# Kernel tuning notes

Hardware: AMD Instinct MI355X
Metric: run time of the kernel (lower is better)

## Reference

```python
import jax, jax.numpy as jnp
import numpy as np

B, T, D = 2, 2048, 1024
H, DK = 16, 64          # num_heads, head_dim (expand_v=1 -> d_v == d_k)
K = 4                    # short conv kernel size
EPS = 1e-5               # gated RMSNorm eps


def setup_inputs() -> dict:
    key = jax.random.key(0)
    ks = jax.random.split(key, 12)
    s = lambda d: d ** -0.5
    return {
        "x": jax.random.normal(ks[0], (B, T, D), jnp.float32),
        "Wq": jax.random.normal(ks[1], (D, H * DK), jnp.float32) * s(D),
        "Wk": jax.random.normal(ks[2], (D, H * DK), jnp.float32) * s(D),
        "Wv": jax.random.normal(ks[3], (D, H * DK), jnp.float32) * s(D),
        "Wa": jax.random.normal(ks[4], (D, H), jnp.float32) * s(D),
        "Wb": jax.random.normal(ks[5], (D, H), jnp.float32) * s(D),
        "Wg": jax.random.normal(ks[6], (D, H * DK), jnp.float32) * s(D),
        "Wo": jax.random.normal(ks[7], (H * DK, D), jnp.float32) * s(H * DK),
        "conv_q": jax.random.normal(ks[8], (H * DK, K), jnp.float32) * s(K),
        "conv_k": jax.random.normal(ks[9], (H * DK, K), jnp.float32) * s(K),
        "conv_v": jax.random.normal(ks[10], (H * DK, K), jnp.float32) * s(K),
        "A_log": jnp.log(jax.random.uniform(ks[11], (H,), jnp.float32, 1.0, 16.0)),
        "dt_bias": jnp.full((H,), 0.5, jnp.float32),
        "rms_w": jnp.ones((DK,), jnp.float32),
    }


def _short_conv(x, w):
    # causal depthwise conv1d (no bias) + silu; x: [B,T,C], w: [C,K]
    kk = w.shape[1]
    xp = jnp.pad(x, ((0, 0), (kk - 1, 0), (0, 0))).transpose(0, 2, 1)  # [B,C,T+K-1]
    y = jax.lax.conv_general_dilated(xp, w[:, None, :], (1,), 'VALID',
                                     feature_group_count=w.shape[0])
    return jax.nn.silu(y.transpose(0, 2, 1))


def _l2norm(x):
    return x * jax.lax.rsqrt(jnp.sum(x * x, -1, keepdims=True) + 1e-6)


def _gated_delta_rule(q, k, v, g, beta):
    # q,k,v: [B,T,H,Dk], g,beta: [B,T,H]; gated delta-rule linear attention
    scale = q.shape[-1] ** -0.5
    q = _l2norm(q) * scale
    k = _l2norm(k)
    qs, ks_, vs, gs, bs = (jnp.moveaxis(a, 1, 0) for a in (q, k, v, g, beta))
    h0 = jnp.zeros((q.shape[0], q.shape[2], q.shape[3], v.shape[3]), q.dtype)

    def step(h, t):
        qt, kt, vt, gt, bt = t
        h = h * jnp.exp(gt)[..., None, None]                      # decay state
        v_adj = (vt - jnp.einsum('bhk,bhkv->bhv', kt, h)) * bt[..., None]
        h = h + kt[..., None] * v_adj[:, :, None, :]              # rank-1 delta update
        ot = jnp.einsum('bhk,bhkv->bhv', qt, h)
        return h, ot

    _, o = jax.lax.scan(step, h0, (qs, ks_, vs, gs, bs))
    return jnp.moveaxis(o, 0, 1)  # [B,T,H,Dv]


def reference(x, Wq, Wk, Wv, Wa, Wb, Wg, Wo, conv_q, conv_k, conv_v, A_log, dt_bias, rms_w):
    q = _short_conv(x @ Wq, conv_q).reshape(B, T, H, DK)
    k = _short_conv(x @ Wk, conv_k).reshape(B, T, H, DK)
    v = _short_conv(x @ Wv, conv_v).reshape(B, T, H, DK)
    g = -jnp.exp(A_log) * jax.nn.softplus(x @ Wa + dt_bias)   # [B,T,H] log-decay
    beta = jax.nn.sigmoid(x @ Wb)                             # [B,T,H]
    o = _gated_delta_rule(q, k, v, g, beta)                   # [B,T,H,DK]
    gate = (x @ Wg).reshape(B, T, H, DK)
    o = o * jax.lax.rsqrt(jnp.mean(o * o, -1, keepdims=True) + EPS) * rms_w
    o = o * jax.nn.silu(gate)                                 # gated RMSNorm
    return o.reshape(B, T, H * DK) @ Wo
```

## Files before the change

### kernel.cpp

```cpp
#include <hip/hip_runtime.h>
#include <hip/hip_bf16.h>
#include <math.h>
#include <stdint.h>

#define BB 2
#define TT 2048
#define DD 1024
#define HH 16
#define DK 64
#define HD 1024
#define NC 32
#define CL 64
#define PAD 68
#define VS 16

typedef short bf16x8 __attribute__((ext_vector_type(8)));
typedef float f32x4 __attribute__((ext_vector_type(4)));
typedef unsigned short u16x8 __attribute__((ext_vector_type(8)));
typedef unsigned short u16x4 __attribute__((ext_vector_type(4)));

#define GAS __attribute__((address_space(1)))
#define LAS __attribute__((address_space(3)))

#define DOT4(a, b) ((a).x*(b).x + (a).y*(b).y + (a).z*(b).z + (a).w*(b).w)

#define OUT16(acc, kf, wv) \
    acc[0][0] += kf.x * wv.x; acc[0][1] += kf.x * wv.y; acc[0][2] += kf.x * wv.z; acc[0][3] += kf.x * wv.w; \
    acc[1][0] += kf.y * wv.x; acc[1][1] += kf.y * wv.y; acc[1][2] += kf.y * wv.z; acc[1][3] += kf.y * wv.w; \
    acc[2][0] += kf.z * wv.x; acc[2][1] += kf.z * wv.y; acc[2][2] += kf.z * wv.z; acc[2][3] += kf.z * wv.w; \
    acc[3][0] += kf.w * wv.x; acc[3][1] += kf.w * wv.y; acc[3][2] += kf.w * wv.z; acc[3][3] += kf.w * wv.w;

#define WSUB(c, hv) \
    acc[0][0] -= wa0.c * hv.x; acc[0][1] -= wa0.c * hv.y; acc[0][2] -= wa0.c * hv.z; acc[0][3] -= wa0.c * hv.w; \
    acc[1][0] -= wa1.c * hv.x; acc[1][1] -= wa1.c * hv.y; acc[1][2] -= wa1.c * hv.z; acc[1][3] -= wa1.c * hv.w; \
    acc[2][0] -= wa2.c * hv.x; acc[2][1] -= wa2.c * hv.y; acc[2][2] -= wa2.c * hv.z; acc[2][3] -= wa2.c * hv.w; \
    acc[3][0] -= wa3.c * hv.x; acc[3][1] -= wa3.c * hv.y; acc[3][2] -= wa3.c * hv.z; acc[3][3] -= wa3.c * hv.w;

#define ACC16(c, wv) \
    acc[0][0] += sa0.c * wv.x; acc[0][1] += sa0.c * wv.y; acc[0][2] += sa0.c * wv.z; acc[0][3] += sa0.c * wv.w; \
    acc[1][0] += sa1.c * wv.x; acc[1][1] += sa1.c * wv.y; acc[1][2] += sa1.c * wv.z; acc[1][3] += sa1.c * wv.w; \
    acc[2][0] += sa2.c * wv.x; acc[2][1] += sa2.c * wv.y; acc[2][2] += sa2.c * wv.z; acc[2][3] += sa2.c * wv.w; \
    acc[3][0] += sa3.c * wv.x; acc[3][1] += sa3.c * wv.y; acc[3][2] += sa3.c * wv.z; acc[3][3] += sa3.c * wv.w;

__device__ __forceinline__ float sigmoidf_(float x) { return 1.0f / (1.0f + expf(-x)); }
__device__ __forceinline__ float siluf_(float x) { return x * sigmoidf_(x); }

__device__ __forceinline__ unsigned short f2bf(float f) {
    unsigned int u = __builtin_bit_cast(unsigned int, f);
    u = (u + 0x7fffu + ((u >> 16) & 1u)) >> 16;
    return (unsigned short)u;
}

__global__ __launch_bounds__(256) void castx_k(const float* __restrict__ src,
                                               unsigned short* __restrict__ dst) {
    const size_t idx = (size_t)blockIdx.x * 256 + threadIdx.x;
    float4 a = *(const float4*)&src[idx * 8];
    float4 b = *(const float4*)&src[idx * 8 + 4];
    u16x8 o;
    o[0] = f2bf(a.x); o[1] = f2bf(a.y); o[2] = f2bf(a.z); o[3] = f2bf(a.w);
    o[4] = f2bf(b.x); o[5] = f2bf(b.y); o[6] = f2bf(b.z); o[7] = f2bf(b.w);
    *(u16x8*)&dst[idx * 8] = o;
}

__global__ __launch_bounds__(256) void castw_k(const float* __restrict__ W,
                                               unsigned short* __restrict__ Wt) {
    __shared__ float t_s[64][65];
    const int tid = threadIdx.x;
    const int rr = tid >> 4;
    const int cc = tid & 15;
    const int r0 = blockIdx.y * 64;
    const int c0 = blockIdx.x * 64;
#pragma unroll
    for (int i = 0; i < 4; ++i) {
        const int row = rr + i * 16;
        float4 v = *(const float4*)&W[(size_t)(r0 + row) * 1024 + c0 + cc * 4];
        t_s[row][cc * 4 + 0] = v.x;
        t_s[row][cc * 4 + 1] = v.y;
        t_s[row][cc * 4 + 2] = v.z;
        t_s[row][cc * 4 + 3] = v.w;
    }
    __syncthreads();
#pragma unroll
    for (int i = 0; i < 4; ++i) {
        const int nr = rr + i * 16;
        u16x4 o;
#pragma unroll
        for (int d = 0; d < 4; ++d) o[d] = f2bf(t_s[cc * 4 + d][nr]);
        *(u16x4*)&Wt[(size_t)(c0 + nr) * 1024 + r0 + cc * 4] = o;
    }
}

__global__ __launch_bounds__(256) void tw_k(const float* __restrict__ Wa,
                                            const float* __restrict__ Wb,
                                            float* __restrict__ Wt) {
    const int o = blockIdx.x;
    const int h = o & 15;
    const float* W = (o < 16) ? Wa : Wb;
    const int tid = threadIdx.x;
    float4 v;
    v.x = W[(size_t)(tid * 4 + 0) * HH + h];
    v.y = W[(size_t)(tid * 4 + 1) * HH + h];
    v.z = W[(size_t)(tid * 4 + 2) * HH + h];
    v.w = W[(size_t)(tid * 4 + 3) * HH + h];
    *(float4*)&Wt[(size_t)o * DD + tid * 4] = v;
}

__global__ __launch_bounds__(256) void gemm_bf16_k(const unsigned short* __restrict__ A,
                                                   const unsigned short* __restrict__ Bt,
                                                   float* __restrict__ C,
                                                   int M, int N, int Kd) {
    __shared__ unsigned short a_s[128 * 32];
    __shared__ unsigned short b_s[128 * 32];

    const int tid = threadIdx.x;
    const int wave = tid >> 6;
    const int lane = tid & 63;
    const int m0 = blockIdx.y * 128;
    const int n0 = blockIdx.x * 128;

    const int quad = lane >> 4;
    const int l16 = lane & 15;
    const int wr = wave >> 1;
    const int wc = wave & 1;

    const int srow = lane >> 2;
    const int sseg = lane & 3;

    f32x4 acc[4][4];
#pragma unroll
    for (int i = 0; i < 4; ++i)
#pragma unroll
        for (int j = 0; j < 4; ++j) acc[i][j] = (f32x4){0.f, 0.f, 0.f, 0.f};

    for (int k0 = 0; k0 < Kd; k0 += 32) {
        __syncthreads();
#pragma unroll
        for (int c = 0; c < 2; ++c) {
            const int region = wave * 2 + c;
            const int r0t = region * 16;
            const int ra = r0t + srow;
            const unsigned short* ga = A + (size_t)(m0 + ra) * Kd + k0 + sseg * 8;
            const unsigned short* gb = Bt + (size_t)(n0 + ra) * Kd + k0 + sseg * 8;
            __builtin_amdgcn_global_load_lds((const GAS unsigned int*)ga,
                                             (LAS unsigned int*)&a_s[r0t * 32], 16, 0, 0);
            __builtin_amdgcn_global_load_lds((const GAS unsigned int*)gb,
                                             (LAS unsigned int*)&b_s[r0t * 32], 16, 0, 0);
        }
        __syncthreads();

        bf16x8 af[4], bfr[4];
#pragma unroll
        for (int i = 0; i < 4; ++i)
            af[i] = *(const bf16x8*)&a_s[(wr * 64 + i * 16 + l16) * 32 + quad * 8];
#pragma unroll
        for (int j = 0; j < 4; ++j)
            bfr[j] = *(const bf16x8*)&b_s[(wc * 64 + j * 16 + l16) * 32 + quad * 8];
#pragma unroll
        for (int i = 0; i < 4; ++i)
#pragma unroll
            for (int j = 0; j < 4; ++j)
                acc[i][j] = __builtin_amdgcn_mfma_f32_16x16x32_bf16(af[i], bfr[j], acc[i][j], 0, 0, 0);
    }

#pragma unroll
    for (int i = 0; i < 4; ++i)
#pragma unroll
        for (int j = 0; j < 4; ++j) {
            const int col = n0 + wc * 64 + j * 16 + l16;
#pragma unroll
            for (int r = 0; r < 4; ++r) {
                const int row = m0 + wr * 64 + i * 16 + quad * 4 + r;
                C[(size_t)row * N + col] = acc[i][j][r];
            }
        }
}

__global__ __launch_bounds__(256) void gemm_qkvg_k(const unsigned short* __restrict__ A,
                                                   const unsigned short* __restrict__ Bt,
                                                   float* __restrict__ Oq,
                                                   float* __restrict__ Ok,
                                                   float* __restrict__ Ov,
                                                   float* __restrict__ Og) {
    __shared__ unsigned short a_s[128 * 32];
    __shared__ unsigned short b_s[128 * 32];

    const int tid = threadIdx.x;
    const int wave = tid >> 6;
    const int lane = tid & 63;
    const int m0 = blockIdx.y * 128;
    const int n0 = blockIdx.x * 128;

    const int quad = lane >> 4;
    const int l16 = lane & 15;
    const int wr = wave >> 1;
    const int wc = wave & 1;

    const int srow = lane >> 2;
    const int sseg = lane & 3;

    f32x4 acc[4][4];
#pragma unroll
    for (int i = 0; i < 4; ++i)
#pragma unroll
        for (int j = 0; j < 4; ++j) acc[i][j] = (f32x4){0.f, 0.f, 0.f, 0.f};

    for (int k0 = 0; k0 < DD; k0 += 32) {
        __syncthreads();
#pragma unroll
        for (int c = 0; c < 2; ++c) {
            const int region = wave * 2 + c;
            const int r0t = region * 16;
            const int ra = r0t + srow;
            const unsigned short* ga = A + (size_t)(m0 + ra) * DD + k0 + sseg * 8;
            const unsigned short* gb = Bt + (size_t)(n0 + ra) * DD + k0 + sseg * 8;
            __builtin_amdgcn_global_load_lds((const GAS unsigned int*)ga,
                                             (LAS unsigned int*)&a_s[r0t * 32], 16, 0, 0);
            __builtin_amdgcn_global_load_lds((const GAS unsigned int*)gb,
                                             (LAS unsigned int*)&b_s[r0t * 32], 16, 0, 0);
        }
        __syncthreads();

        bf16x8 af[4], bfr[4];
#pragma unroll
        for (int i = 0; i < 4; ++i)
            af[i] = *(const bf16x8*)&a_s[(wr * 64 + i * 16 + l16) * 32 + quad * 8];
#pragma unroll
        for (int j = 0; j < 4; ++j)
            bfr[j] = *(const bf16x8*)&b_s[(wc * 64 + j * 16 + l16) * 32 + quad * 8];
#pragma unroll
        for (int i = 0; i < 4; ++i)
#pragma unroll
            for (int j = 0; j < 4; ++j)
                acc[i][j] = __builtin_amdgcn_mfma_f32_16x16x32_bf16(af[i], bfr[j], acc[i][j], 0, 0, 0);
    }

    float* Cd = (n0 < 1024) ? Oq : (n0 < 2048) ? Ok : (n0 < 3072) ? Ov : Og;
    const int nl = n0 & 1023;
#pragma unroll
    for (int i = 0; i < 4; ++i)
#pragma unroll
        for (int j = 0; j < 4; ++j) {
            const int col = nl + wc * 64 + j * 16 + l16;
#pragma unroll
            for (int r = 0; r < 4; ++r) {
                const int row = m0 + wr * 64 + i * 16 + quad * 4 + r;
                Cd[(size_t)row * HD + col] = acc[i][j][r];
            }
        }
}

__global__ __launch_bounds__(256) void gbeta_k(const float* __restrict__ x,
                                               const float* __restrict__ Wt,
                                               const float* __restrict__ A_log,
                                               const float* __restrict__ dt_bias,
                                               float* __restrict__ g,
                                               float* __restrict__ beta) {
    __shared__ __align__(16) float xs[8][DD];
    const int r0 = blockIdx.x * 8;
    const int tid = threadIdx.x;

#pragma unroll
    for (int i = 0; i < 8; ++i) {
        const int f = tid + i * 256;
        const int r = f >> 8;
        const int col = (f & 255) * 4;
        *(float4*)&xs[r][col] = *(const float4*)&x[((size_t)r0 + r) * DD + col];
    }
    __syncthreads();

    const int out = tid >> 3;
    const int part = tid & 7;
    const int h = out & 15;
    const float* Wrow = Wt + (size_t)out * DD;

    float a0 = 0, a1 = 0, a2 = 0, a3 = 0, a4 = 0, a5 = 0, a6 = 0, a7 = 0;
#pragma unroll 4
    for (int i = 0; i < 32; ++i) {
        const int d = i * 32 + part * 4;
        const float4 wv = *(const float4*)&Wrow[d];
        float4 x0 = *(const float4*)&xs[0][d];
        float4 x1 = *(const float4*)&xs[1][d];
        float4 x2 = *(const float4*)&xs[2][d];
        float4 x3 = *(const float4*)&xs[3][d];
        float4 x4 = *(const float4*)&xs[4][d];
        float4 x5 = *(const float4*)&xs[5][d];
        float4 x6 = *(const float4*)&xs[6][d];
        float4 x7 = *(const float4*)&xs[7][d];
        a0 += DOT4(x0, wv); a1 += DOT4(x1, wv);
        a2 += DOT4(x2, wv); a3 += DOT4(x3, wv);
        a4 += DOT4(x4, wv); a5 += DOT4(x5, wv);
        a6 += DOT4(x6, wv); a7 += DOT4(x7, wv);
    }
#pragma unroll
    for (int s = 1; s <= 4; s <<= 1) {
        a0 += __shfl_xor(a0, s); a1 += __shfl_xor(a1, s);
        a2 += __shfl_xor(a2, s); a3 += __shfl_xor(a3, s);
        a4 += __shfl_xor(a4, s); a5 += __shfl_xor(a5, s);
        a6 += __shfl_xor(a6, s); a7 += __shfl_xor(a7, s);
    }

    if (part == 0) {
        float sv[8] = {a0, a1, a2, a3, a4, a5, a6, a7};
        if (out < 16) {
            const float ae = -expf(A_log[h]);
            const float db = dt_bias[h];
#pragma unroll
            for (int r = 0; r < 8; ++r) {
                float v = sv[r] + db;
                float sp = (v > 20.0f) ? v : log1pf(expf(v));
                g[((size_t)r0 + r) * HH + h] = ae * sp;
            }
        } else {
#pragma unroll
            for (int r = 0; r < 8; ++r)
                beta[((size_t)r0 + r) * HH + h] = sigmoidf_(sv[r]);
        }
    }
}

__global__ __launch_bounds__(64) void stage_k(const float* __restrict__ q_pre,
                                              const float* __restrict__ k_pre,
                                              const float* __restrict__ cq,
                                              const float* __restrict__ ck,
                                              const float* __restrict__ g,
                                              float* __restrict__ Qc,
                                              float* __restrict__ Kc,
                                              float* __restrict__ bcum) {
    const int blk = blockIdx.x;
    const int bh = blk >> 5;
    const int c = blk & 31;
    const int b = bh >> 4;
    const int h = bh & 15;
    const int lane = threadIdx.x;
    const int ch = h * DK + lane;

    const float4 wq4 = *(const float4*)&cq[ch * 4];
    const float4 wk4 = *(const float4*)&ck[ch * 4];

    float qw0 = 0, qw1 = 0, qw2 = 0, kw0 = 0, kw1 = 0, kw2 = 0;
    {
        const int t0 = c * CL;
        if (t0 - 3 >= 0) { size_t bi = ((size_t)b * TT + t0 - 3) * HD + ch; qw0 = q_pre[bi]; kw0 = k_pre[bi]; }
        if (t0 - 2 >= 0) { size_t bi = ((size_t)b * TT + t0 - 2) * HD + ch; qw1 = q_pre[bi]; kw1 = k_pre[bi]; }
        if (t0 - 1 >= 0) { size_t bi = ((size_t)b * TT + t0 - 1) * HD + ch; qw2 = q_pre[bi]; kw2 = k_pre[bi]; }
    }
    float* Qo = Qc + (size_t)blk * 4096;
    float* Ko = Kc + (size_t)blk * 4096;

    for (int tt = 0; tt < CL; ++tt) {
        const int t = c * CL + tt;
        const size_t bi = ((size_t)b * TT + t) * HD + ch;
        const float qc_ = q_pre[bi];
        const float kc_ = k_pre[bi];
        float qa = qw0 * wq4.x + qw1 * wq4.y + qw2 * wq4.z + qc_ * wq4.w;
        float ka = kw0 * wk4.x + kw1 * wk4.y + kw2 * wk4.z + kc_ * wk4.w;
        qw0 = qw1; qw1 = qw2; qw2 = qc_;
        kw0 = kw1; kw1 = kw2; kw2 = kc_;
        qa = siluf_(qa);
        ka = siluf_(ka);
        float qs2 = qa * qa, ks2 = ka * ka;
#pragma unroll
        for (int s = 32; s > 0; s >>= 1) {
            qs2 += __shfl_xor(qs2, s);
            ks2 += __shfl_xor(ks2, s);
        }
        Qo[tt * 64 + lane] = qa * rsqrtf(qs2 + 1e-6f) * 0.125f;
        Ko[tt * 64 + lane] = ka * rsqrtf(ks2 + 1e-6f);
    }

    float cum = g[((size_t)b * TT + c * CL + lane) * HH + h];
#pragma unroll
    for (int s = 1; s < 64; s <<= 1) {
        float u = __shfl_up(cum, s);
        if (lane >= s) cum += u;
    }
    bcum[(size_t)blk * 64 + lane] = cum;
}

__global__ __launch_bounds__(256) void prep_k(const float* __restrict__ Kc,
                                              const float* __restrict__ v_pre,
                                              const float* __restrict__ cv,
                                              const float* __restrict__ bcum,
                                              const float* __restrict__ bbuf,
                                              float* __restrict__ Wv,
                                              float* __restrict__ Wk) {
    __shared__ __align__(16) float k_s[CL * PAD];
    __shared__ __align__(16) float wv_s[CL * PAD];
    __shared__ __align__(16) float wk_s[CL * PAD];
    __shared__ __align__(16) float A_s[CL * PAD];
    __shared__ float T_s[4][16 * 17];
    __shared__ float b_s[CL], beta_s[CL], bk_s[CL];

    const int blk = blockIdx.x;
    const int bh = blk >> 5;
    const int c = blk & 31;
    const int b = bh >> 4;
    const int h = bh & 15;
    const int tid = threadIdx.x;

    if (tid < 64) {
        float bv = bcum[(size_t)blk * 64 + tid];
        float be = bbuf[((size_t)b * TT + c * CL + tid) * HH + h];
        b_s[tid] = bv;
        beta_s[tid] = be;
        bk_s[tid] = be * __expf(bv);
    }
    __syncthreads();

    {
        const float4* Kg = (const float4*)(Kc + (size_t)blk * 4096);
#pragma unroll
        for (int i = 0; i < 4; ++i) {
            int f = tid + i * 256;
            int t = f >> 4;
            int d = t * PAD + (f & 15) * 4;
            float4 kv = Kg[f];
            *(float4*)&k_s[d] = kv;
            float sk = bk_s[t];
            *(float4*)&wk_s[d] = make_float4(kv.x * sk, kv.y * sk, kv.z * sk, kv.w * sk);
        }
    }

    {
        const int lane = tid & 63;
        const int q4 = tid >> 6;
        const int ch = h * DK + lane;
        const float4 wv4 = *(const float4*)&cv[ch * 4];
        const int T0 = c * CL + q4 * 16;
        float w0 = 0, w1 = 0, w2 = 0;
        if (T0 - 3 >= 0) w0 = v_pre[((size_t)b * TT + T0 - 3) * HD + ch];
        if (T0 - 2 >= 0) w1 = v_pre[((size_t)b * TT + T0 - 2) * HD + ch];
        if (T0 - 1 >= 0) w2 = v_pre[((size_t)b * TT + T0 - 1) * HD + ch];
#pragma unroll 1
        for (int i = 0; i < 16; ++i) {
            const int t = T0 + i;
            const float vc_ = v_pre[((size_t)b * TT + t) * HD + ch];
            float va = w0 * wv4.x + w1 * wv4.y + w2 * wv4.z + vc_ * wv4.w;
            w0 = w1; w1 = w2; w2 = vc_;
            va = siluf_(va);
            wv_s[(q4 * 16 + i) * PAD + lane] = va * beta_s[q4 * 16 + i];
        }
    }
    __syncthreads();

    {
        const int t0 = (tid >> 4) * 4, s0 = (tid & 15) * 4;
        float acc[4][4] = {};
        for (int kk = 0; kk < 64; kk += 4) {
            float4 ta0 = *(const float4*)&k_s[(t0 + 0) * PAD + kk];
            float4 ta1 = *(const float4*)&k_s[(t0 + 1) * PAD + kk];
            float4 ta2 = *(const float4*)&k_s[(t0 + 2) * PAD + kk];
            float4 ta3 = *(const float4*)&k_s[(t0 + 3) * PAD + kk];
            float4 sb0 = *(const float4*)&k_s[(s0 + 0) * PAD + kk];
            float4 sb1 = *(const float4*)&k_s[(s0 + 1) * PAD + kk];
            float4 sb2 = *(const float4*)&k_s[(s0 + 2) * PAD + kk];
            float4 sb3 = *(const float4*)&k_s[(s0 + 3) * PAD + kk];
            acc[0][0] += DOT4(ta0, sb0); acc[0][1] += DOT4(ta0, sb1);
            acc[0][2] += DOT4(ta0, sb2); acc[0][3] += DOT4(ta0, sb3);
            acc[1][0] += DOT4(ta1, sb0); acc[1][1] += DOT4(ta1, sb1);
            acc[1][2] += DOT4(ta1, sb2); acc[1][3] += DOT4(ta1, sb3);
            acc[2][0] += DOT4(ta2, sb0); acc[2][1] += DOT4(ta2, sb1);
            acc[2][2] += DOT4(ta2, sb2); acc[2][3] += DOT4(ta2, sb3);
            acc[3][0] += DOT4(ta3, sb0); acc[3][1] += DOT4(ta3, sb1);
            acc[3][2] += DOT4(ta3, sb2); acc[3][3] += DOT4(ta3, sb3);
        }
#pragma unroll
        for (int i = 0; i < 4; ++i)
#pragma unroll
            for (int j = 0; j < 4; ++j) {
                const int t = t0 + i, s = s0 + j;
                A_s[t * PAD + s] = (s < t) ? acc[i][j] * beta_s[t] * __expf(b_s[t] - b_s[s]) : 0.0f;
            }
    }
    __syncthreads();

    if (tid < 64) {
        const int d = tid >> 4;
        const int col = tid & 15;
        const int base = d * 16;
        float tcol[16];
#pragma unroll
        for (int s = 0; s < 16; ++s) tcol[s] = (s == col) ? 1.0f : 0.0f;
#pragma unroll
        for (int t = 1; t < 16; ++t) {
            float a = 0.0f;
#pragma unroll
            for (int s = 0; s < 16; ++s)
                if (s < t) a += A_s[(base + t) * PAD + base + s] * tcol[s];
            tcol[t] -= a;
        }
#pragma unroll
        for (int t = 0; t < 16; ++t) T_s[d][t * 17 + col] = tcol[t];
    }
    __syncthreads();

    {
        const int r = tid >> 4;
        const int cg = tid & 15;
        float* Wc = (cg < 8) ? wv_s : wk_s;
        const int cc = (cg & 7) * 8;

        for (int tb = 0; tb < 4; ++tb) {
            const int t = tb * 16 + r;
            if (tb > 0) {
                float4 lo = *(const float4*)&Wc[t * PAD + cc];
                float4 hi = *(const float4*)&Wc[t * PAD + cc + 4];
#pragma unroll 4
                for (int s = 0; s < tb * 16; ++s) {
                    const float a = A_s[t * PAD + s];
                    float4 wlo = *(const float4*)&Wc[s * PAD + cc];
                    float4 whi = *(const float4*)&Wc[s * PAD + cc + 4];
                    lo.x -= a * wlo.x; lo.y -= a * wlo.y; lo.z -= a * wlo.z; lo.w -= a * wlo.w;
                    hi.x -= a * whi.x; hi.y -= a * whi.y; hi.z -= a * whi.z; hi.w -= a * whi.w;
                }
                *(float4*)&Wc[t * PAD + cc] = lo;
                *(float4*)&Wc[t * PAD + cc + 4] = hi;
            }
            __syncthreads();
            float4 alo = make_float4(0, 0, 0, 0);
            float4 ahi = make_float4(0, 0, 0, 0);
#pragma unroll 4
            for (int s = 0; s < 16; ++s) {
                const float tv = T_s[tb][r * 17 + s];
                float4 wlo = *(const float4*)&Wc[(tb * 16 + s) * PAD + cc];
                float4 whi = *(const float4*)&Wc[(tb * 16 + s) * PAD + cc + 4];
                alo.x += tv * wlo.x; alo.y += tv * wlo.y; alo.z += tv * wlo.z; alo.w += tv * wlo.w;
                ahi.x += tv * whi.x; ahi.y += tv * whi.y; ahi.z += tv * whi.z; ahi.w += tv * whi.w;
            }
            __syncthreads();
            *(float4*)&Wc[t * PAD + cc] = alo;
            *(float4*)&Wc[t * PAD + cc + 4] = ahi;
            __syncthreads();
        }
    }

    float4* Wvg = (float4*)(Wv + (size_t)blk * 4096);
    float4* Wkg = (float4*)(Wk + (size_t)blk * 4096);
#pragma unroll
    for (int i = 0; i < 4; ++i) {
        int f = tid + i * 256;
        int d = (f >> 4) * PAD + (f & 15) * 4;
        Wvg[f] = *(float4*)&wv_s[d];
        Wkg[f] = *(float4*)&wk_s[d];
    }
}

__global__ __launch_bounds__(256) void ab_k(const float* __restrict__ Kc,
                                            const float* __restrict__ Wv,
                                            const float* __restrict__ Wk,
                                            const float* __restrict__ bcum,
                                            float* __restrict__ Ab,
                                            float* __restrict__ Bb) {
    __shared__ __align__(16) float kt_s[CL * PAD];
    __shared__ __align__(16) float wk_s[CL * PAD];
    __shared__ __align__(16) float wv_s[CL * PAD];
    __shared__ float e_s[CL];
    __shared__ float ebC_s;

    const int blk = blockIdx.x;
    const int tid = threadIdx.x;

    if (tid < 64) {
        float bC = bcum[(size_t)blk * 64 + 63];
        e_s[tid] = __expf(bC - bcum[(size_t)blk * 64 + tid]);
        if (tid == 63) ebC_s = __expf(bC);
    }
    __syncthreads();

    {
        const float4* Kg = (const float4*)(Kc + (size_t)blk * 4096);
        const float4* Wkg = (const float4*)(Wk + (size_t)blk * 4096);
        const float4* Wvg = (const float4*)(Wv + (size_t)blk * 4096);
#pragma unroll
        for (int i = 0; i < 4; ++i) {
            int f = tid + i * 256;
            int t = f >> 4;
            int d = t * PAD + (f & 15) * 4;
            float4 kv = Kg[f];
            float e = e_s[t];
            *(float4*)&kt_s[d] = make_float4(kv.x * e, kv.y * e, kv.z * e, kv.w * e);
            *(float4*)&wk_s[d] = Wkg[f];
            *(float4*)&wv_s[d] = Wvg[f];
        }
    }
    __syncthreads();

    const int k0 = (tid >> 4) * 4, m0 = (tid & 15) * 4;
    float aA[4][4] = {};
    float aB[4][4] = {};
    for (int ss = 0; ss < 64; ss += 4) {
        float4 kf0 = *(const float4*)&kt_s[(ss + 0) * PAD + k0];
        float4 kf1 = *(const float4*)&kt_s[(ss + 1) * PAD + k0];
        float4 kf2 = *(const float4*)&kt_s[(ss + 2) * PAD + k0];
        float4 kf3 = *(const float4*)&kt_s[(ss + 3) * PAD + k0];
        float4 wa0 = *(const float4*)&wk_s[(ss + 0) * PAD + m0];
        float4 wa1 = *(const float4*)&wk_s[(ss + 1) * PAD + m0];
        float4 wa2 = *(const float4*)&wk_s[(ss + 2) * PAD + m0];
        float4 wa3 = *(const float4*)&wk_s[(ss + 3) * PAD + m0];
        float4 wb0 = *(const float4*)&wv_s[(ss + 0) * PAD + m0];
        float4 wb1 = *(const float4*)&wv_s[(ss + 1) * PAD + m0];
        float4 wb2 = *(const float4*)&wv_s[(ss + 2) * PAD + m0];
        float4 wb3 = *(const float4*)&wv_s[(ss + 3) * PAD + m0];
        OUT16(aA, kf0, wa0); OUT16(aA, kf1, wa1); OUT16(aA, kf2, wa2); OUT16(aA, kf3, wa3);
        OUT16(aB, kf0, wb0); OUT16(aB, kf1, wb1); OUT16(aB, kf2, wb2); OUT16(aB, kf3, wb3);
    }

    const float ebC = ebC_s;
    float* Ag = Ab + (size_t)blk * 4096;
    float* Bg = Bb + (size_t)blk * 4096;
#pragma unroll
    for (int i = 0; i < 4; ++i) {
        const int kk = k0 + i;
        float4 av = make_float4(-aA[i][0], -aA[i][1], -aA[i][2], -aA[i][3]);
        if (kk - m0 == 0) av.x += ebC;
        if (kk - m0 == 1) av.y += ebC;
        if (kk - m0 == 2) av.z += ebC;
        if (kk - m0 == 3) av.w += ebC;
        *(float4*)&Ag[kk * 64 + m0] = av;
        *(float4*)&Bg[kk * 64 + m0] = make_float4(aB[i][0], aB[i][1], aB[i][2], aB[i][3]);
    }
}

__global__ __launch_bounds__(64, 1) void hrec_k(const float* __restrict__ Ab,
                                                const float* __restrict__ Bb,
                                                float* __restrict__ Hst) {
    const int blk = blockIdx.x;
    const int bh = blk & 31;
    const int vs = blk >> 5;
    const int k = threadIdx.x;

    __shared__ float h_s[4][64];
#pragma unroll
    for (int j = 0; j < 4; ++j) h_s[j][k] = 0.0f;

    float h0 = 0, h1 = 0, h2 = 0, h3 = 0;

    const float* Abase = Ab + (size_t)bh * NC * 4096 + k * 64;
    const float* Bbase = Bb + (size_t)bh * NC * 4096 + k * 64 + vs * 4;

    float4 an[16];
#pragma unroll
    for (int q = 0; q < 16; ++q) an[q] = *(const float4*)&Abase[q * 4];
    float4 bn = *(const float4*)&Bbase[0];
    __syncthreads();

    for (int c = 0; c < NC; ++c) {
        float4 ac[16];
#pragma unroll
        for (int q = 0; q < 16; ++q) ac[q] = an[q];
        float4 b0 = bn;
        if (c + 1 < NC) {
            const float* An = Abase + (size_t)(c + 1) * 4096;
            const float* Bn = Bbase + (size_t)(c + 1) * 4096;
#pragma unroll
            for (int q = 0; q < 16; ++q) an[q] = *(const float4*)&An[q * 4];
            bn = *(const float4*)&Bn[0];
        }

        float* Hg = Hst + ((size_t)bh * NC + c) * 4096 + k * 64 + vs * 4;
        *(float4*)&Hg[0] = make_float4(h0, h1, h2, h3);

        float a0 = b0.x, a1 = b0.y, a2 = b0.z, a3 = b0.w;
#pragma unroll
        for (int m4 = 0; m4 < 16; ++m4) {
            float4 av = ac[m4];
            float4 hv0 = *(const float4*)&h_s[0][m4 * 4];
            float4 hv1 = *(const float4*)&h_s[1][m4 * 4];
            float4 hv2 = *(const float4*)&h_s[2][m4 * 4];
            float4 hv3 = *(const float4*)&h_s[3][m4 * 4];
            a0 += DOT4(av, hv0); a1 += DOT4(av, hv1);
            a2 += DOT4(av, hv2); a3 += DOT4(av, hv3);
        }
        __syncthreads();
        h0 = a0; h1 = a1; h2 = a2; h3 = a3;
        h_s[0][k] = h0; h_s[1][k] = h1; h_s[2][k] = h2; h_s[3][k] = h3;
        __syncthreads();
    }
}

__global__ __launch_bounds__(256) void wfix_k(const float* __restrict__ Wk,
                                              const float* __restrict__ Hst,
                                              float* __restrict__ Wio) {
    __shared__ __align__(16) float wk_s[CL * PAD];
    __shared__ __align__(16) float h_s[CL * PAD];

    const int blk = blockIdx.x;
    const int tid = threadIdx.x;

    {
        const float4* Wkg = (const float4*)(Wk + (size_t)blk * 4096);
        const float4* Hg = (const float4*)(Hst + (size_t)blk * 4096);
#pragma unroll
        for (int i = 0; i < 4; ++i) {
            int f = tid + i * 256;
            int d = (f >> 4) * PAD + (f & 15) * 4;
            *(float4*)&wk_s[d] = Wkg[f];
            *(float4*)&h_s[d] = Hg[f];
        }
    }
    __syncthreads();

    const int t0 = (tid >> 4) * 4, v0 = (tid & 15) * 4;
    float* Wg = Wio + (size_t)blk * 4096;

    float acc[4][4];
#pragma unroll
    for (int i = 0; i < 4; ++i) {
        float4 wv = *(const float4*)&Wg[(t0 + i) * 64 + v0];
        acc[i][0] = wv.x; acc[i][1] = wv.y; acc[i][2] = wv.z; acc[i][3] = wv.w;
    }
    for (int kk = 0; kk < 64; kk += 4) {
        float4 wa0 = *(const float4*)&wk_s[(t0 + 0) * PAD + kk];
        float4 wa1 = *(const float4*)&wk_s[(t0 + 1) * PAD + kk];
        float4 wa2 = *(const float4*)&wk_s[(t0 + 2) * PAD + kk];
        float4 wa3 = *(const float4*)&wk_s[(t0 + 3) * PAD + kk];
        float4 hb0 = *(const float4*)&h_s[(kk + 0) * PAD + v0];
        float4 hb1 = *(const float4*)&h_s[(kk + 1) * PAD + v0];
        float4 hb2 = *(const float4*)&h_s[(kk + 2) * PAD + v0];
        float4 hb3 = *(const float4*)&h_s[(kk + 3) * PAD + v0];
        WSUB(x, hb0); WSUB(y, hb1); WSUB(z, hb2); WSUB(w, hb3);
    }
#pragma unroll
    for (int i = 0; i < 4; ++i)
        *(float4*)&Wg[(t0 + i) * 64 + v0] =
            make_float4(acc[i][0], acc[i][1], acc[i][2], acc[i][3]);
}

__global__ __launch_bounds__(256) void out_k(const float* __restrict__ Qc,
                                             const float* __restrict__ Kc,
                                             const float* __restrict__ Wb_,
                                             const float* __restrict__ Hst,
                                             const float* __restrict__ bcum,
                                             float* __restrict__ o_scan) {
    __shared__ __align__(16) float q_s[CL * PAD];
    __shared__ __align__(16) float s_s[CL * PAD];
    __shared__ __align__(16) float h_s[CL * PAD];
    __shared__ __align__(16) float w_s[CL * PAD];
    __shared__ float b_s[64];

    const int blk = blockIdx.x;
    const int bh = blk >> 5;
    const int c = blk & 31;
    const int b = bh >> 4;
    const int h = bh & 15;
    const int tid = threadIdx.x;

    if (tid < 64) b_s[tid] = bcum[(size_t)blk * 64 + tid];
    {
        const float4* Qg = (const float4*)(Qc + (size_t)blk * 4096);
        const float4* Kg = (const float4*)(Kc + (size_t)blk * 4096);
        const float4* Hg = (const float4*)(Hst + (size_t)blk * 4096);
        const float4* Wg = (const float4*)(Wb_ + (size_t)blk * 4096);
#pragma unroll
        for (int i = 0; i < 4; ++i) {
            int f = tid + i * 256;
            int d = (f >> 4) * PAD + (f & 15) * 4;
            *(float4*)&q_s[d] = Qg[f];
            *(float4*)&s_s[d] = Kg[f];
            *(float4*)&h_s[d] = Hg[f];
            *(float4*)&w_s[d] = Wg[f];
        }
    }
    __syncthreads();

    {
        const int t0 = (tid >> 4) * 4, s0 = (tid & 15) * 4;
        float acc[4][4] = {};
        for (int kk = 0; kk < 64; kk += 4) {
            float4 ta0 = *(const float4*)&q_s[(t0 + 0) * PAD + kk];
            float4 ta1 = *(const float4*)&q_s[(t0 + 1) * PAD + kk];
            float4 ta2 = *(const float4*)&q_s[(t0 + 2) * PAD + kk];
            float4 ta3 = *(const float4*)&q_s[(t0 + 3) * PAD + kk];
            float4 sb0 = *(const float4*)&s_s[(s0 + 0) * PAD + kk];
            float4 sb1 = *(const float4*)&s_s[(s0 + 1) * PAD + kk];
            float4 sb2 = *(const float4*)&s_s[(s0 + 2) * PAD + kk];
            float4 sb3 = *(const float4*)&s_s[(s0 + 3) * PAD + kk];
            acc[0][0] += DOT4(ta0, sb0); acc[0][1] += DOT4(ta0, sb1);
            acc[0][2] += DOT4(ta0, sb2); acc[0][3] += DOT4(ta0, sb3);
            acc[1][0] += DOT4(ta1, sb0); acc[1][1] += DOT4(ta1, sb1);
            acc[1][2] += DOT4(ta1, sb2); acc[1][3] += DOT4(ta1, sb3);
            acc[2][0] += DOT4(ta2, sb0); acc[2][1] += DOT4(ta2, sb1);
            acc[2][2] += DOT4(ta2, sb2); acc[2][3] += DOT4(ta2, sb3);
            acc[3][0] += DOT4(ta3, sb0); acc[3][1] += DOT4(ta3, sb1);
            acc[3][2] += DOT4(ta3, sb2); acc[3][3] += DOT4(ta3, sb3);
        }
        __syncthreads();
#pragma unroll
        for (int i = 0; i < 4; ++i)
#pragma unroll
            for (int j = 0; j < 4; ++j) {
                const int t = t0 + i, s = s0 + j;
                s_s[t * PAD + s] = (s <= t) ? acc[i][j] * __expf(b_s[t] - b_s[s]) : 0.0f;
            }
    }
#pragma unroll
    for (int i = 0; i < 16; ++i) {
        const int e = tid + i * 256;
        const int t = e >> 6;
        q_s[t * PAD + (e & 63)] *= __expf(b_s[t]);
    }
    __syncthreads();

    {
        const int t0 = (tid >> 4) * 4, v0 = (tid & 15) * 4;
        float acc[4][4] = {};
        for (int ss = 0; ss < 64; ss += 4) {
            float4 sa0 = *(const float4*)&s_s[(t0 + 0) * PAD + ss];
            float4 sa1 = *(const float4*)&s_s[(t0 + 1) * PAD + ss];
            float4 sa2 = *(const float4*)&s_s[(t0 + 2) * PAD + ss];
            float4 sa3 = *(const float4*)&s_s[(t0 + 3) * PAD + ss];
            float4 wb0 = *(const float4*)&w_s[(ss + 0) * PAD + v0];
            float4 wb1 = *(const float4*)&w_s[(ss + 1) * PAD + v0];
            float4 wb2 = *(const float4*)&w_s[(ss + 2) * PAD + v0];
            float4 wb3 = *(const float4*)&w_s[(ss + 3) * PAD + v0];
            ACC16(x, wb0); ACC16(y, wb1); ACC16(z, wb2); ACC16(w, wb3);
        }
        for (int kk = 0; kk < 64; kk += 4) {
            float4 sa0 = *(const float4*)&q_s[(t0 + 0) * PAD + kk];
            float4 sa1 = *(const float4*)&q_s[(t0 + 1) * PAD + kk];
            float4 sa2 = *(const float4*)&q_s[(t0 + 2) * PAD + kk];
            float4 sa3 = *(const float4*)&q_s[(t0 + 3) * PAD + kk];
            float4 wb0 = *(const float4*)&h_s[(kk + 0) * PAD + v0];
            float4 wb1 = *(const float4*)&h_s[(kk + 1) * PAD + v0];
            float4 wb2 = *(const float4*)&h_s[(kk + 2) * PAD + v0];
            float4 wb3 = *(const float4*)&h_s[(kk + 3) * PAD + v0];
            ACC16(x, wb0); ACC16(y, wb1); ACC16(z, wb2); ACC16(w, wb3);
        }
#pragma unroll
        for (int i = 0; i < 4; ++i) {
            const int t = c * CL + t0 + i;
            *(float4*)&o_scan[(((size_t)b * TT + t) * HH + h) * DK + v0] =
                make_float4(acc[i][0], acc[i][1], acc[i][2], acc[i][3]);
        }
    }
}

__global__ __launch_bounds__(256) void gnorm_k(const float* __restrict__ o_scan,
                                               const float* __restrict__ gate,
                                               const float* __restrict__ rms_w,
                                               unsigned short* __restrict__ o2) {
    const int tid = threadIdx.x;
    const int grp = tid >> 6;
    const int lane = tid & 63;
    const int bth = blockIdx.x * 4 + grp;
    const int h = bth & 15;
    const int row = bth >> 4;

    float ov = o_scan[(size_t)bth * DK + lane];
    float s = ov * ov;
#pragma unroll
    for (int sh = 32; sh > 0; sh >>= 1) s += __shfl_xor(s, sh);
    float r = rsqrtf(s * (1.0f / 64.0f) + 1e-5f);

    float gt = gate[(size_t)row * HD + h * DK + lane];
    o2[(size_t)row * HD + h * DK + lane] = f2bf(ov * r * rms_w[lane] * siluf_(gt));
}

extern "C" void kernel_launch(void* const* d_in, const int* in_sizes, int n_in,
                              void* d_out, int out_size, void* d_ws, size_t ws_size,
                              hipStream_t stream) {
    (void)in_sizes; (void)n_in; (void)out_size; (void)ws_size;

    const float* x       = (const float*)d_in[0];
    const float* Wq      = (const float*)d_in[1];
    const float* Wk_     = (const float*)d_in[2];
    const float* Wv_     = (const float*)d_in[3];
    const float* Wa      = (const float*)d_in[4];
    const float* Wb      = (const float*)d_in[5];
    const float* Wg      = (const float*)d_in[6];
    const float* Wo      = (const float*)d_in[7];
    const float* conv_q  = (const float*)d_in[8];
    const float* conv_k  = (const float*)d_in[9];
    const float* conv_v  = (const float*)d_in[10];
    const float* A_log   = (const float*)d_in[11];
    const float* dt_bias = (const float*)d_in[12];
    const float* rms_w   = (const float*)d_in[13];
    float* out = (float*)d_out;

    float* ws = (float*)d_ws;
    const size_t NTOK = (size_t)BB * TT;
    const size_t BIG = NTOK * HD;

    float* q_pre = ws + 0 * BIG;
    float* k_pre = ws + 1 * BIG;
    float* v_pre = ws + 2 * BIG;
    float* gatep = ws + 3 * BIG;
    float* Qc    = ws + 4 * BIG;
    float* Kc    = ws + 5 * BIG;
    float* gbuf  = ws + 6 * BIG;
    float* bbuf  = gbuf + NTOK * HH;
    float* bcumb = bbuf + NTOK * HH;

    unsigned short* xb  = (unsigned short*)(bcumb + NTOK * HH);
    unsigned short* wqt = xb + (size_t)NTOK * DD;
    unsigned short* wkt = wqt + (size_t)DD * HD;
    unsigned short* wvt = wkt + (size_t)DD * HD;
    unsigned short* wgt = wvt + (size_t)DD * HD;
    unsigned short* wot = wgt + (size_t)DD * HD;

    float* Bbuf = (float*)(wot + (size_t)DD * HD);
    float* HstB = Bbuf + BIG;
    float* Wabt = HstB + BIG;

    float* Wvb    = q_pre;
    float* Wkb    = k_pre;
    float* Abuf   = v_pre;
    float* o_scan = v_pre;
    unsigned short* o2b = (unsigned short*)Qc;

    castx_k<<<(int)(NTOK * DD / (256 * 8)), 256, 0, stream>>>(x, xb);
    dim3 tg(16, 16);
    castw_k<<<tg, 256, 0, stream>>>(Wq, wqt);
    castw_k<<<tg, 256, 0, stream>>>(Wk_, wkt);
    castw_k<<<tg, 256, 0, stream>>>(Wv_, wvt);
    castw_k<<<tg, 256, 0, stream>>>(Wg, wgt);
    castw_k<<<tg, 256, 0, stream>>>(Wo, wot);
    tw_k<<<32, 256, 0, stream>>>(Wa, Wb, Wabt);

    gemm_qkvg_k<<<dim3(32, 32), 256, 0, stream>>>(xb, wqt, q_pre, k_pre, v_pre, gatep);

    gbeta_k<<<(int)(NTOK / 8), 256, 0, stream>>>(x, Wabt, A_log, dt_bias, gbuf, bbuf);

    stage_k<<<BB * HH * NC, 64, 0, stream>>>(q_pre, k_pre, conv_q, conv_k, gbuf,
                                             Qc, Kc, bcumb);

    prep_k<<<BB * HH * NC, 256, 0, stream>>>(Kc, v_pre, conv_v, bcumb, bbuf, Wvb, Wkb);

    ab_k<<<BB * HH * NC, 256, 0, stream>>>(Kc, Wvb, Wkb, bcumb, Abuf, Bbuf);
    hrec_k<<<BB * HH * VS, 64, 0, stream>>>(Abuf, Bbuf, HstB);
    wfix_k<<<BB * HH * NC, 256, 0, stream>>>(Wkb, HstB, Wvb);

    out_k<<<BB * HH * NC, 256, 0, stream>>>(Qc, Kc, Wvb, HstB, bcumb, o_scan);

    gnorm_k<<<(int)(NTOK * HH / 4), 256, 0, stream>>>(o_scan, gatep, rms_w, o2b);

    gemm_bf16_k<<<dim3(HD / 128, NTOK / 128), 256, 0, stream>>>(o2b, wot, out,
                                                                (int)NTOK, HD, DD);
}
```

Baseline: 476.0 us.

## Double-buffer chunk transition matrices in LDS via async global-to-LDS loads

The serial chunk-state recurrence kernel now streams each chunk's 64x64 A matrix into a double-buffered LDS area with global_load_lds, replacing the 64-float4 register prefetch. Manual vmcnt/lgkmcnt waits replace the workgroup barriers, which is valid because the block is a single 64-lane wave. The producer kernel writes A in an interleaved layout so each lane's 16-byte load is contiguous, and a barrier is added before the A_s writes in another kernel. The aim is lower register pressure and less barrier latency on the sequential critical path. The cost is hand-counted wait thresholds that become fragile if the instruction ordering changes.

```diff
diff --git a/kernel.cpp b/kernel.cpp
--- a/kernel.cpp
+++ b/kernel.cpp
@@ -464,6 +464,7 @@
             acc[3][0] += DOT4(ta3, sb0); acc[3][1] += DOT4(ta3, sb1);
             acc[3][2] += DOT4(ta3, sb2); acc[3][3] += DOT4(ta3, sb3);
         }
+        __syncthreads();
 #pragma unroll
         for (int i = 0; i < 4; ++i)
 #pragma unroll
@@ -608,6 +609,7 @@
     const float ebC = ebC_s;
     float* Ag = Ab + (size_t)blk * 4096;
     float* Bg = Bb + (size_t)blk * 4096;
+    const int p = tid & 15;
 #pragma unroll
     for (int i = 0; i < 4; ++i) {
         const int kk = k0 + i;
@@ -616,54 +618,62 @@
         if (kk - m0 == 1) av.y += ebC;
         if (kk - m0 == 2) av.z += ebC;
         if (kk - m0 == 3) av.w += ebC;
-        *(float4*)&Ag[kk * 64 + m0] = av;
+        *(float4*)&Ag[p * 256 + kk * 4] = av;
         *(float4*)&Bg[kk * 64 + m0] = make_float4(aB[i][0], aB[i][1], aB[i][2], aB[i][3]);
     }
 }
 
-__global__ __launch_bounds__(64, 1) void hrec_k(const float* __restrict__ Ab,
-                                                const float* __restrict__ Bb,
-                                                float* __restrict__ Hst) {
+__global__ __launch_bounds__(64) void hrec_k(const float* __restrict__ Ab,
+                                             const float* __restrict__ Bb,
+                                             float* __restrict__ Hst) {
     const int blk = blockIdx.x;
     const int bh = blk & 31;
     const int vs = blk >> 5;
     const int k = threadIdx.x;
 
-    __shared__ float h_s[4][64];
+    __shared__ __align__(16) float A_lds[2][4096];
+    __shared__ __align__(16) float h_s[4][64];
+
 #pragma unroll
     for (int j = 0; j < 4; ++j) h_s[j][k] = 0.0f;
-
     float h0 = 0, h1 = 0, h2 = 0, h3 = 0;
 
-    const float* Abase = Ab + (size_t)bh * NC * 4096 + k * 64;
+    const float* Abase = Ab + (size_t)bh * NC * 4096;
     const float* Bbase = Bb + (size_t)bh * NC * 4096 + k * 64 + vs * 4;
-
-    float4 an[16];
-#pragma unroll
-    for (int q = 0; q < 16; ++q) an[q] = *(const float4*)&Abase[q * 4];
+    float* Hbase = Hst + (size_t)bh * NC * 4096 + k * 64 + vs * 4;
+
+#pragma unroll
+    for (int i = 0; i < 16; ++i)
+        __builtin_amdgcn_global_load_lds((const GAS unsigned int*)(Abase + i * 256 + k * 4),
+                                         (LAS unsigned int*)&A_lds[0][i * 256], 16, 0, 0);
     float4 bn = *(const float4*)&Bbase[0];
-    __syncthreads();
-
+
+    const float* Acur = &A_lds[0][0];
+    float* Anxt = &A_lds[1][0];
+
+#pragma unroll 1
     for (int c = 0; c < NC; ++c) {
-        float4 ac[16];
-#pragma unroll
-        for (int q = 0; q < 16; ++q) ac[q] = an[q];
         float4 b0 = bn;
+
+        *(float4*)&Hbase[(size_t)c * 4096] = make_float4(h0, h1, h2, h3);
+
         if (c + 1 < NC) {
             const float* An = Abase + (size_t)(c + 1) * 4096;
-            const float* Bn = Bbase + (size_t)(c + 1) * 4096;
-#pragma unroll
-            for (int q = 0; q < 16; ++q) an[q] = *(const float4*)&An[q * 4];
-            bn = *(const float4*)&Bn[0];
-        }
-
-        float* Hg = Hst + ((size_t)bh * NC + c) * 4096 + k * 64 + vs * 4;
-        *(float4*)&Hg[0] = make_float4(h0, h1, h2, h3);
+#pragma unroll
+            for (int i = 0; i < 16; ++i)
+                __builtin_amdgcn_global_load_lds((const GAS unsigned int*)(An + i * 256 + k * 4),
+                                                 (LAS unsigned int*)&Anxt[i * 256], 16, 0, 0);
+            bn = *(const float4*)&Bbase[(size_t)(c + 1) * 4096];
+            asm volatile("s_waitcnt vmcnt(18)" ::: "memory");
+        } else {
+            asm volatile("s_waitcnt vmcnt(1)" ::: "memory");
+        }
+        __builtin_amdgcn_sched_barrier(0);
 
         float a0 = b0.x, a1 = b0.y, a2 = b0.z, a3 = b0.w;
 #pragma unroll
         for (int m4 = 0; m4 < 16; ++m4) {
-            float4 av = ac[m4];
+            float4 av = *(const float4*)&Acur[m4 * 256 + k * 4];
             float4 hv0 = *(const float4*)&h_s[0][m4 * 4];
             float4 hv1 = *(const float4*)&h_s[1][m4 * 4];
             float4 hv2 = *(const float4*)&h_s[2][m4 * 4];
@@ -671,10 +681,11 @@
             a0 += DOT4(av, hv0); a1 += DOT4(av, hv1);
             a2 += DOT4(av, hv2); a3 += DOT4(av, hv3);
         }
-        __syncthreads();
         h0 = a0; h1 = a1; h2 = a2; h3 = a3;
         h_s[0][k] = h0; h_s[1][k] = h1; h_s[2][k] = h2; h_s[3][k] = h3;
-        __syncthreads();
+        asm volatile("s_waitcnt lgkmcnt(0)" ::: "memory");
+
+        const float* t = Acur; Acur = Anxt; Anxt = (float*)t;
     }
 }
 
```

Measured after the change: 464.2 us. -2.5%, faster.
